# Kernel optimization log

Hardware: AMD Instinct MI355X
Metric: run time of the kernel (lower is better)

## Reference

```python
import jax, jax.numpy as jnp
import numpy as np

WINDOW_SIZE = 5


def setup_inputs() -> dict:
    key = jax.random.key(0)
    x = jax.random.normal(key, (16, 2048, 512), dtype=jnp.float32)
    return {"x": x}


def reference(x) -> jnp.ndarray:
    # x: [B, T, D]. Output: [B, T, D*W] where slot i holds x shifted left by i,
    # zero-padded past the end of the sequence.
    B, T, D = x.shape
    W = WINDOW_SIZE
    # Pad W-1 zero timesteps at the end, matching tf.concat([x, zeros], axis=1).
    xp = jnp.pad(x, ((0, 0), (0, W - 1), (0, 0)))  # [B, T+W-1, D]
    # Shift-i view is xp[:, i:i+T, :]; concatenate along feature axis.
    windows = [xp[:, i:i + T, :] for i in range(W)]  # W x [B, T, D]
    return jnp.concatenate(windows, axis=2)  # [B, T, D*W]
```

## Files before the change

kernel.cpp:

```cpp
#include <hip/hip_runtime.h>


typedef float f4 __attribute__((ext_vector_type(4)));

constexpr int T_DIM = 2048;
constexpr int D4 = 128;
constexpr int W = 5;
constexpr int R = 16;
constexpr int SROWS = R + W - 1;
constexpr int ROW_OUT = W * D4;

__global__ __launch_bounds__(256) void window_embed_kernel(
    const f4* __restrict__ x, f4* __restrict__ out) {
  __shared__ f4 lds[SROWS * D4];

  const int tchunk = blockIdx.x;
  const int b = blockIdx.y;
  const int t0 = tchunk * R;
  const int tid = threadIdx.x;

  const long long in_base = ((long long)b * T_DIM + t0) * D4;
#pragma unroll
  for (int k = 0; k < SROWS * D4 / 256; ++k) {
    int f = k * 256 + tid;
    int r = f >> 7;
    f4 v = (f4)0.f;
    if (t0 + r < T_DIM) v = x[in_base + f];
    lds[f] = v;
  }
  __syncthreads();

  const long long out_base = ((long long)b * T_DIM + t0) * ROW_OUT;
#pragma unroll 2
  for (int ii = 0; ii < R; ii += 2) {
#pragma unroll
    for (int q = 0; q < 5; ++q) {
      int o = q * 256 + tid;
      int hi = (o >= ROW_OUT) ? 1 : 0;
      f4 v = lds[ii * D4 + o - hi * 512];
      __builtin_nontemporal_store(
          v, &out[out_base + (long long)(ii + hi) * ROW_OUT + (o - hi * ROW_OUT)]);
    }
  }
}

extern "C" void kernel_launch(void* const* d_in, const int* in_sizes, int n_in,
                              void* d_out, int out_size, void* d_ws, size_t ws_size,
                              hipStream_t stream) {
  const f4* x = (const f4*)d_in[0];
  f4* out = (f4*)d_out;

  dim3 grid(T_DIM / R, 16);
  window_embed_kernel<<<grid, 256, 0, stream>>>(x, out);
}
```

Measured before the change: 72.88 us.

## Replace LDS staging with direct per-row global loads and doubled rows per block

Drops the shared-memory tile and __syncthreads. Each thread now loads its W shifted input rows straight from global memory, relying on L1/L2 for reuse, and streams them to the output with nontemporal stores. Rows per block grow from 16 to 32, which halves the grid size, and each half of the block covers a contiguous group of rows. This removes the LDS round trip and the barrier, but each input element is now read from cache about W times, and fewer blocks may lower occupancy.

```diff
diff --git a/kernel.cpp b/kernel.cpp
--- a/kernel.cpp
+++ b/kernel.cpp
@@ -6,40 +6,34 @@
 constexpr int T_DIM = 2048;
 constexpr int D4 = 128;
 constexpr int W = 5;
-constexpr int R = 16;
-constexpr int SROWS = R + W - 1;
+constexpr int R = 32;
 constexpr int ROW_OUT = W * D4;
 
 __global__ __launch_bounds__(256) void window_embed_kernel(
     const f4* __restrict__ x, f4* __restrict__ out) {
-  __shared__ f4 lds[SROWS * D4];
+  const int tid  = threadIdx.x;
+  const int lane = tid & 127;
+  const int half = tid >> 7;
 
-  const int tchunk = blockIdx.x;
-  const int b = blockIdx.y;
-  const int t0 = tchunk * R;
-  const int tid = threadIdx.x;
+  const int t0 = blockIdx.x * R;
+  const long long row0 = (long long)blockIdx.y * T_DIM + t0;
 
-  const long long in_base = ((long long)b * T_DIM + t0) * D4;
+  const f4* __restrict__ xb = x + row0 * D4 + lane;
+  f4* __restrict__ ob = out + row0 * (long long)ROW_OUT + lane;
+
+  const f4 zero = (f4)0.f;
+
+#pragma unroll 4
+  for (int i = 0; i < R / 2; ++i) {
+    const int r = half * (R / 2) + i;
+    f4 v[W];
 #pragma unroll
-  for (int k = 0; k < SROWS * D4 / 256; ++k) {
-    int f = k * 256 + tid;
-    int r = f >> 7;
-    f4 v = (f4)0.f;
-    if (t0 + r < T_DIM) v = x[in_base + f];
-    lds[f] = v;
-  }
-  __syncthreads();
-
-  const long long out_base = ((long long)b * T_DIM + t0) * ROW_OUT;
-#pragma unroll 2
-  for (int ii = 0; ii < R; ii += 2) {
+    for (int q = 0; q < W; ++q) {
+      v[q] = (t0 + r + q < T_DIM) ? xb[(r + q) * D4] : zero;
+    }
 #pragma unroll
-    for (int q = 0; q < 5; ++q) {
-      int o = q * 256 + tid;
-      int hi = (o >= ROW_OUT) ? 1 : 0;
-      f4 v = lds[ii * D4 + o - hi * 512];
-      __builtin_nontemporal_store(
-          v, &out[out_base + (long long)(ii + hi) * ROW_OUT + (o - hi * ROW_OUT)]);
+    for (int q = 0; q < W; ++q) {
+      __builtin_nontemporal_store(v[q], &ob[(long long)r * ROW_OUT + q * D4]);
     }
   }
 }
```

Result: faster. 70.08 us, median of 2 (-3.8%).
